# Optimization experiments

Measured on AMD Instinct MI355X. Metric: run time of the kernel, lower is better.

## Reference

```python
import jax, jax.numpy as jnp
import numpy as np

H = 32  # hidden_size

def _lstm_cell(x, h, c, Wih, Whh, bih, bhh):
    # PyTorch LSTMCell: gates order i, f, g, o
    g = x @ Wih.T + bih + h @ Whh.T + bhh  # [B, 4H]
    i, f, gg, o = jnp.split(g, 4, axis=-1)
    i = jax.nn.sigmoid(i); f = jax.nn.sigmoid(f)
    gg = jnp.tanh(gg);     o = jax.nn.sigmoid(o)
    c_new = f * c + i * gg
    h_new = o * jnp.tanh(c_new)
    return h_new, c_new


def setup_inputs() -> dict:
    key = jax.random.key(0)
    ks = jax.random.split(key, 16)
    B, T, I = 16384, 32, 27
    s_ih0 = 1.0 / np.sqrt(H)
    inp = {
        "obscured_tensor": jax.random.uniform(ks[0], (B, T, I), dtype=jnp.float32),
        "guessed_tensor": jax.random.uniform(ks[1], (B, 26), dtype=jnp.float32),
        # init_state uses xavier_normal on [B,H]: std = sqrt(2/(B+H))
        "h0": jax.random.normal(ks[2], (B, H), dtype=jnp.float32) * np.sqrt(2.0 / (B + H)),
        "c0": jax.random.normal(ks[3], (B, H), dtype=jnp.float32) * np.sqrt(2.0 / (B + H)),
        # layer 0 LSTMCell params (uniform(-1/sqrt(H), 1/sqrt(H)) like torch)
        "Wih0": jax.random.uniform(ks[4], (4 * H, I), jnp.float32, -s_ih0, s_ih0),
        "Whh0": jax.random.uniform(ks[5], (4 * H, H), jnp.float32, -s_ih0, s_ih0),
        "bih0": jax.random.uniform(ks[6], (4 * H,), jnp.float32, -s_ih0, s_ih0),
        "bhh0": jax.random.uniform(ks[7], (4 * H,), jnp.float32, -s_ih0, s_ih0),
        # layer 1 LSTMCell params
        "Wih1": jax.random.uniform(ks[8], (4 * H, H), jnp.float32, -s_ih0, s_ih0),
        "Whh1": jax.random.uniform(ks[9], (4 * H, H), jnp.float32, -s_ih0, s_ih0),
        "bih1": jax.random.uniform(ks[10], (4 * H,), jnp.float32, -s_ih0, s_ih0),
        "bhh1": jax.random.uniform(ks[11], (4 * H,), jnp.float32, -s_ih0, s_ih0),
        # fc: Linear(H + 26, 26)
        "Wfc": jax.random.uniform(ks[12], (26, H + 26), jnp.float32, -1.0 / np.sqrt(H + 26), 1.0 / np.sqrt(H + 26)),
        "bfc": jax.random.uniform(ks[13], (26,), jnp.float32, -1.0 / np.sqrt(H + 26), 1.0 / np.sqrt(H + 26)),
    }
    return inp


def reference(obscured_tensor, guessed_tensor, h0, c0,
              Wih0, Whh0, bih0, bhh0, Wih1, Whh1, bih1, bhh1, Wfc, bfc):
    B, T, _ = obscured_tensor.shape
    # faithful to torch: .view(T, B, -1) is a raw reshape, not a transpose
    xs = obscured_tensor.reshape(T, B, -1)  # [T, B, 27]

    def step(carry, x):
        h1, c1, h2, c2, hsum = carry
        h1, c1 = _lstm_cell(x, h1, c1, Wih0, Whh0, bih0, bhh0)
        h2, c2 = _lstm_cell(h1, h2, c2, Wih1, Whh1, bih1, bhh1)
        return (h1, c1, h2, c2, hsum + h2), None

    # init_state aliases the same xavier-initialized tensor for all layers
    init = (h0, c0, h0, c0, jnp.zeros_like(h0))
    (h1, c1, h2, c2, hsum), _ = jax.lax.scan(step, init, xs)

    # 'avg' aggregation: mean over time of concat(h_top, guessed);
    # guessed is time-constant so mean(concat) == concat(mean(h), guessed)
    agg = jnp.concatenate([hsum / T, guessed_tensor], axis=1)  # [B, H+26]
    logits = agg @ Wfc.T + bfc
    return logits, jax.nn.sigmoid(logits)
```

## Files before the change

kernel.cpp:

```cpp
#include <hip/hip_runtime.h>
#include <hip/hip_bf16.h>

#define NB 16384
#define NT 32
#define NI 27
#define NH 32
#define NG 26

typedef __attribute__((ext_vector_type(8))) short bf16x8;
typedef __attribute__((ext_vector_type(4))) float f32x4;
typedef __attribute__((ext_vector_type(4))) int   i32x4;

#define MFMA(a, b, c) __builtin_amdgcn_mfma_f32_16x16x32_bf16((a), (b), (c), 0, 0, 0)

static __device__ __forceinline__ int pack2(float lo, float hi) {
    unsigned short a = __builtin_bit_cast(unsigned short, __float2bfloat16(lo));
    unsigned short b = __builtin_bit_cast(unsigned short, __float2bfloat16(hi));
    return (int)(((unsigned)b << 16) | (unsigned)a);
}

static __device__ __forceinline__ float sigm(float x) {
    return __builtin_amdgcn_rcpf(1.0f + __expf(-x));
}
static __device__ __forceinline__ float tanh_(float x) {
    return 2.0f * __builtin_amdgcn_rcpf(1.0f + __expf(-2.0f * x)) - 1.0f;
}

static __device__ __forceinline__ bf16x8 load_wfrag(const float* __restrict__ W,
                                                    int rowlen, int nrows, int row, int k0) {
    int w[4];
#pragma unroll
    for (int q = 0; q < 4; ++q) {
        int k = k0 + 2 * q;
        float lo = (row < nrows && k     < rowlen) ? W[row * rowlen + k]     : 0.0f;
        float hi = (row < nrows && k + 1 < rowlen) ? W[row * rowlen + k + 1] : 0.0f;
        w[q] = pack2(lo, hi);
    }
    i32x4 v = { w[0], w[1], w[2], w[3] };
    return __builtin_bit_cast(bf16x8, v);
}

static __device__ __forceinline__ bf16x8 redist(const float hn[4][2], int a0, int a1, bool mhi) {
    int w00 = pack2(hn[0][0], hn[1][0]);
    int w01 = pack2(hn[2][0], hn[3][0]);
    int w10 = pack2(hn[0][1], hn[1][1]);
    int w11 = pack2(hn[2][1], hn[3][1]);
    int q0lo = __builtin_amdgcn_ds_bpermute(a0, w00), q0hi = __builtin_amdgcn_ds_bpermute(a0, w10);
    int q1lo = __builtin_amdgcn_ds_bpermute(a0, w01), q1hi = __builtin_amdgcn_ds_bpermute(a0, w11);
    int q2lo = __builtin_amdgcn_ds_bpermute(a1, w00), q2hi = __builtin_amdgcn_ds_bpermute(a1, w10);
    int q3lo = __builtin_amdgcn_ds_bpermute(a1, w01), q3hi = __builtin_amdgcn_ds_bpermute(a1, w11);
    i32x4 v = { mhi ? q0hi : q0lo, mhi ? q1hi : q1lo, mhi ? q2hi : q2lo, mhi ? q3hi : q3lo };
    return __builtin_bit_cast(bf16x8, v);
}

__global__ __launch_bounds__(256, 1)
void lstm_mfma(const float* __restrict__ X,
               const float* __restrict__ Gu,
               const float* __restrict__ H0, const float* __restrict__ C0,
               const float* __restrict__ Wih0, const float* __restrict__ Whh0,
               const float* __restrict__ bih0, const float* __restrict__ bhh0,
               const float* __restrict__ Wih1, const float* __restrict__ Whh1,
               const float* __restrict__ bih1, const float* __restrict__ bhh1,
               const float* __restrict__ Wfc, const float* __restrict__ bfc,
               float* __restrict__ out)
{
    const int lane = threadIdx.x & 63;
    const int bl   = lane & 15;
    const int g4   = lane >> 4;
    const int k0   = 8 * g4;
    const int wid  = blockIdx.x * (blockDim.x >> 6) + (threadIdx.x >> 6);
    const int batch = wid * 16 + bl;
    const bool mhi = (g4 >> 1) != 0;
    const int a0 = 4 * (bl + 16 * (2 * (g4 & 1)));
    const int a1 = a0 + 64;

    bf16x8 A0x[8], A0h[8], A1i[8], A1h[8];
    f32x4  b0[8], b1[8];
#pragma unroll
    for (int m = 0; m < 8; ++m) {
        A0x[m] = load_wfrag(Wih0, NI, 4 * NH, 16 * m + bl, k0);
        A0h[m] = load_wfrag(Whh0, NH, 4 * NH, 16 * m + bl, k0);
        A1i[m] = load_wfrag(Wih1, NH, 4 * NH, 16 * m + bl, k0);
        A1h[m] = load_wfrag(Whh1, NH, 4 * NH, 16 * m + bl, k0);
#pragma unroll
        for (int r = 0; r < 4; ++r) {
            int gr = 16 * m + 4 * g4 + r;
            b0[m][r] = bih0[gr] + bhh0[gr];
            b1[m][r] = bih1[gr] + bhh1[gr];
        }
    }
    bf16x8 Afc0[2], Afc1[2];
#pragma unroll
    for (int m2 = 0; m2 < 2; ++m2) {
        Afc0[m2] = load_wfrag(Wfc, NH + NG, NG, 16 * m2 + bl, k0);
        Afc1[m2] = load_wfrag(Wfc, NH + NG, NG, 16 * m2 + bl, NH + k0);
    }

    const float* h0p = H0 + (size_t)batch * NH;
    const float* c0p = C0 + (size_t)batch * NH;
    int hw[4];
#pragma unroll
    for (int q = 0; q < 4; ++q) hw[q] = pack2(h0p[k0 + 2 * q], h0p[k0 + 2 * q + 1]);
    i32x4 hv = { hw[0], hw[1], hw[2], hw[3] };
    bf16x8 h1f = __builtin_bit_cast(bf16x8, hv);
    bf16x8 h2f = h1f;
    float c1[4][2], c2[4][2], hsum[4][2];
#pragma unroll
    for (int mh = 0; mh < 2; ++mh)
#pragma unroll
        for (int r = 0; r < 4; ++r) {
            float c = c0p[16 * mh + 4 * g4 + r];
            c1[r][mh] = c; c2[r][mh] = c; hsum[r][mh] = 0.0f;
        }

    float xn[8];
    {
        const float* xp = X + ((size_t)0 * NB + batch) * NI;
#pragma unroll
        for (int j = 0; j < 8; ++j) { int k = k0 + j; xn[j] = (k < NI) ? xp[k] : 0.0f; }
    }

#pragma unroll 1
    for (int t = 0; t < NT; ++t) {
        int xw[4];
#pragma unroll
        for (int q = 0; q < 4; ++q) xw[q] = pack2(xn[2 * q], xn[2 * q + 1]);
        i32x4 xv = { xw[0], xw[1], xw[2], xw[3] };
        bf16x8 xf = __builtin_bit_cast(bf16x8, xv);
        if (t + 1 < NT) {
            const float* xp = X + ((size_t)(t + 1) * NB + batch) * NI;
#pragma unroll
            for (int j = 0; j < 8; ++j) { int k = k0 + j; xn[j] = (k < NI) ? xp[k] : 0.0f; }
        }

        f32x4 g[8];
#pragma unroll
        for (int m = 0; m < 8; ++m) g[m] = MFMA(A0x[m], xf, b0[m]);
#pragma unroll
        for (int m = 0; m < 8; ++m) g[m] = MFMA(A0h[m], h1f, g[m]);
        float hn1[4][2];
#pragma unroll
        for (int mh = 0; mh < 2; ++mh)
#pragma unroll
            for (int r = 0; r < 4; ++r) {
                float iv = sigm(g[0 + mh][r]);
                float fv = sigm(g[2 + mh][r]);
                float gv = tanh_(g[4 + mh][r]);
                float ov = sigm(g[6 + mh][r]);
                float c  = fmaf(fv, c1[r][mh], iv * gv);
                c1[r][mh] = c;
                hn1[r][mh] = ov * tanh_(c);
            }
        h1f = redist(hn1, a0, a1, mhi);

#pragma unroll
        for (int m = 0; m < 8; ++m) g[m] = MFMA(A1i[m], h1f, b1[m]);
#pragma unroll
        for (int m = 0; m < 8; ++m) g[m] = MFMA(A1h[m], h2f, g[m]);
        float hn2[4][2];
#pragma unroll
        for (int mh = 0; mh < 2; ++mh)
#pragma unroll
            for (int r = 0; r < 4; ++r) {
                float iv = sigm(g[0 + mh][r]);
                float fv = sigm(g[2 + mh][r]);
                float gv = tanh_(g[4 + mh][r]);
                float ov = sigm(g[6 + mh][r]);
                float c  = fmaf(fv, c2[r][mh], iv * gv);
                c2[r][mh] = c;
                float h = ov * tanh_(c);
                hn2[r][mh] = h;
                hsum[r][mh] += h;
            }
        h2f = redist(hn2, a0, a1, mhi);
    }

    float hs[4][2];
#pragma unroll
    for (int mh = 0; mh < 2; ++mh)
#pragma unroll
        for (int r = 0; r < 4; ++r) hs[r][mh] = hsum[r][mh] * (1.0f / NT);
    bf16x8 hsf = redist(hs, a0, a1, mhi);

    int gw[4];
    {
        const float* gp = Gu + (size_t)batch * NG;
#pragma unroll
        for (int q = 0; q < 4; ++q) {
            int k = k0 + 2 * q;
            float lo = (k     < NG) ? gp[k]     : 0.0f;
            float hi = (k + 1 < NG) ? gp[k + 1] : 0.0f;
            gw[q] = pack2(lo, hi);
        }
    }
    i32x4 gv_ = { gw[0], gw[1], gw[2], gw[3] };
    bf16x8 guf = __builtin_bit_cast(bf16x8, gv_);

    f32x4 zero4 = { 0.0f, 0.0f, 0.0f, 0.0f };
    f32x4 L[2];
#pragma unroll
    for (int m2 = 0; m2 < 2; ++m2) L[m2] = MFMA(Afc0[m2], hsf, zero4);
#pragma unroll
    for (int m2 = 0; m2 < 2; ++m2) L[m2] = MFMA(Afc1[m2], guf, L[m2]);

#pragma unroll
    for (int m2 = 0; m2 < 2; ++m2)
#pragma unroll
        for (int r = 0; r < 4; ++r) {
            int row = 16 * m2 + 4 * g4 + r;
            if (row < NG) {
                float v = L[m2][r] + bfc[row];
                out[(size_t)batch * NG + row] = v;
                out[(size_t)NB * NG + (size_t)batch * NG + row] = sigm(v);
            }
        }
}

extern "C" void kernel_launch(void* const* d_in, const int* in_sizes, int n_in,
                              void* d_out, int out_size, void* d_ws, size_t ws_size,
                              hipStream_t stream) {
    const float* X    = (const float*)d_in[0];
    const float* Gu   = (const float*)d_in[1];
    const float* H0   = (const float*)d_in[2];
    const float* C0   = (const float*)d_in[3];
    const float* Wih0 = (const float*)d_in[4];
    const float* Whh0 = (const float*)d_in[5];
    const float* bih0 = (const float*)d_in[6];
    const float* bhh0 = (const float*)d_in[7];
    const float* Wih1 = (const float*)d_in[8];
    const float* Whh1 = (const float*)d_in[9];
    const float* bih1 = (const float*)d_in[10];
    const float* bhh1 = (const float*)d_in[11];
    const float* Wfc  = (const float*)d_in[12];
    const float* bfc  = (const float*)d_in[13];
    float* out = (float*)d_out;

    dim3 grid(NB / 16 / 4), block(256);
    hipLaunchKernelGGL(lstm_mfma, grid, block, 0, stream,
                       X, Gu, H0, C0, Wih0, Whh0, bih0, bhh0,
                       Wih1, Whh1, bih1, bhh1, Wfc, bfc, out);
}
```

Measured before the change: 77.47 us.

## Split each 16-batch LSTM tile across two waves with LDS exchange

Each 16-row batch tile was handled by one wave computing all 8 gate row-blocks. It is now split across two waves that each compute 4 gate blocks, chosen so every wave holds one i/f/g/o block for its own 16 hidden units. The hidden state is exchanged through shared memory with a __syncthreads per layer per step, replacing the in-wave ds_bpermute redistribution. This doubles the wave count, from 1024 to 2048, and halves the per-wave serial MFMA and activation chain, to expose more parallelism. In exchange it adds block barriers and LDS round-trips on the recurrent critical path.

```diff
diff --git a/kernel.cpp b/kernel.cpp
--- a/kernel.cpp
+++ b/kernel.cpp
@@ -40,61 +40,44 @@
     return __builtin_bit_cast(bf16x8, v);
 }
 
-static __device__ __forceinline__ bf16x8 redist(const float hn[4][2], int a0, int a1, bool mhi) {
-    int w00 = pack2(hn[0][0], hn[1][0]);
-    int w01 = pack2(hn[2][0], hn[3][0]);
-    int w10 = pack2(hn[0][1], hn[1][1]);
-    int w11 = pack2(hn[2][1], hn[3][1]);
-    int q0lo = __builtin_amdgcn_ds_bpermute(a0, w00), q0hi = __builtin_amdgcn_ds_bpermute(a0, w10);
-    int q1lo = __builtin_amdgcn_ds_bpermute(a0, w01), q1hi = __builtin_amdgcn_ds_bpermute(a0, w11);
-    int q2lo = __builtin_amdgcn_ds_bpermute(a1, w00), q2hi = __builtin_amdgcn_ds_bpermute(a1, w10);
-    int q3lo = __builtin_amdgcn_ds_bpermute(a1, w01), q3hi = __builtin_amdgcn_ds_bpermute(a1, w11);
-    i32x4 v = { mhi ? q0hi : q0lo, mhi ? q1hi : q1lo, mhi ? q2hi : q2lo, mhi ? q3hi : q3lo };
-    return __builtin_bit_cast(bf16x8, v);
-}
-
-__global__ __launch_bounds__(256, 1)
-void lstm_mfma(const float* __restrict__ X,
-               const float* __restrict__ Gu,
-               const float* __restrict__ H0, const float* __restrict__ C0,
-               const float* __restrict__ Wih0, const float* __restrict__ Whh0,
-               const float* __restrict__ bih0, const float* __restrict__ bhh0,
-               const float* __restrict__ Wih1, const float* __restrict__ Whh1,
-               const float* __restrict__ bih1, const float* __restrict__ bhh1,
-               const float* __restrict__ Wfc, const float* __restrict__ bfc,
-               float* __restrict__ out)
+__global__ __launch_bounds__(128, 2)
+void lstm_split(const float* __restrict__ X,
+                const float* __restrict__ Gu,
+                const float* __restrict__ H0, const float* __restrict__ C0,
+                const float* __restrict__ Wih0, const float* __restrict__ Whh0,
+                const float* __restrict__ bih0, const float* __restrict__ bhh0,
+                const float* __restrict__ Wih1, const float* __restrict__ Whh1,
+                const float* __restrict__ bih1, const float* __restrict__ bhh1,
+                const float* __restrict__ Wfc, const float* __restrict__ bfc,
+                float* __restrict__ out)
 {
     const int lane = threadIdx.x & 63;
+    const int s    = threadIdx.x >> 6;
     const int bl   = lane & 15;
     const int g4   = lane >> 4;
     const int k0   = 8 * g4;
-    const int wid  = blockIdx.x * (blockDim.x >> 6) + (threadIdx.x >> 6);
-    const int batch = wid * 16 + bl;
-    const bool mhi = (g4 >> 1) != 0;
-    const int a0 = 4 * (bl + 16 * (2 * (g4 & 1)));
-    const int a1 = a0 + 64;
-
-    bf16x8 A0x[8], A0h[8], A1i[8], A1h[8];
-    f32x4  b0[8], b1[8];
-#pragma unroll
-    for (int m = 0; m < 8; ++m) {
-        A0x[m] = load_wfrag(Wih0, NI, 4 * NH, 16 * m + bl, k0);
-        A0h[m] = load_wfrag(Whh0, NH, 4 * NH, 16 * m + bl, k0);
-        A1i[m] = load_wfrag(Wih1, NH, 4 * NH, 16 * m + bl, k0);
-        A1h[m] = load_wfrag(Whh1, NH, 4 * NH, 16 * m + bl, k0);
+    const int batch = blockIdx.x * 16 + bl;
+
+    __shared__ unsigned int hb[2][16][16];
+
+    bf16x8 A0x[4], A0h[4], A1i[4], A1h[4];
+    f32x4  b0[4], b1[4];
+#pragma unroll
+    for (int j = 0; j < 4; ++j) {
+        int m = 2 * j + s;
+        A0x[j] = load_wfrag(Wih0, NI, 4 * NH, 16 * m + bl, k0);
+        A0h[j] = load_wfrag(Whh0, NH, 4 * NH, 16 * m + bl, k0);
+        A1i[j] = load_wfrag(Wih1, NH, 4 * NH, 16 * m + bl, k0);
+        A1h[j] = load_wfrag(Whh1, NH, 4 * NH, 16 * m + bl, k0);
 #pragma unroll
         for (int r = 0; r < 4; ++r) {
             int gr = 16 * m + 4 * g4 + r;
-            b0[m][r] = bih0[gr] + bhh0[gr];
-            b1[m][r] = bih1[gr] + bhh1[gr];
-        }
-    }
-    bf16x8 Afc0[2], Afc1[2];
-#pragma unroll
-    for (int m2 = 0; m2 < 2; ++m2) {
-        Afc0[m2] = load_wfrag(Wfc, NH + NG, NG, 16 * m2 + bl, k0);
-        Afc1[m2] = load_wfrag(Wfc, NH + NG, NG, 16 * m2 + bl, NH + k0);
-    }
+            b0[j][r] = bih0[gr] + bhh0[gr];
+            b1[j][r] = bih1[gr] + bhh1[gr];
+        }
+    }
+    bf16x8 Afc0 = load_wfrag(Wfc, NH + NG, NG, 16 * s + bl, k0);
+    bf16x8 Afc1 = load_wfrag(Wfc, NH + NG, NG, 16 * s + bl, NH + k0);
 
     const float* h0p = H0 + (size_t)batch * NH;
     const float* c0p = C0 + (size_t)batch * NH;
@@ -104,21 +87,21 @@
     i32x4 hv = { hw[0], hw[1], hw[2], hw[3] };
     bf16x8 h1f = __builtin_bit_cast(bf16x8, hv);
     bf16x8 h2f = h1f;
-    float c1[4][2], c2[4][2], hsum[4][2];
-#pragma unroll
-    for (int mh = 0; mh < 2; ++mh)
-#pragma unroll
-        for (int r = 0; r < 4; ++r) {
-            float c = c0p[16 * mh + 4 * g4 + r];
-            c1[r][mh] = c; c2[r][mh] = c; hsum[r][mh] = 0.0f;
-        }
+    float c1[4], c2[4], hsum[4];
+#pragma unroll
+    for (int r = 0; r < 4; ++r) {
+        float c = c0p[16 * s + 4 * g4 + r];
+        c1[r] = c; c2[r] = c; hsum[r] = 0.0f;
+    }
 
     float xn[8];
     {
-        const float* xp = X + ((size_t)0 * NB + batch) * NI;
+        const float* xp = X + (size_t)batch * NI;
 #pragma unroll
         for (int j = 0; j < 8; ++j) { int k = k0 + j; xn[j] = (k < NI) ? xp[k] : 0.0f; }
     }
+
+    const int wr = 8 * s + 2 * g4;
 
 #pragma unroll 1
     for (int t = 0; t < NT; ++t) {
@@ -133,54 +116,52 @@
             for (int j = 0; j < 8; ++j) { int k = k0 + j; xn[j] = (k < NI) ? xp[k] : 0.0f; }
         }
 
-        f32x4 g[8];
-#pragma unroll
-        for (int m = 0; m < 8; ++m) g[m] = MFMA(A0x[m], xf, b0[m]);
-#pragma unroll
-        for (int m = 0; m < 8; ++m) g[m] = MFMA(A0h[m], h1f, g[m]);
-        float hn1[4][2];
-#pragma unroll
-        for (int mh = 0; mh < 2; ++mh)
-#pragma unroll
-            for (int r = 0; r < 4; ++r) {
-                float iv = sigm(g[0 + mh][r]);
-                float fv = sigm(g[2 + mh][r]);
-                float gv = tanh_(g[4 + mh][r]);
-                float ov = sigm(g[6 + mh][r]);
-                float c  = fmaf(fv, c1[r][mh], iv * gv);
-                c1[r][mh] = c;
-                hn1[r][mh] = ov * tanh_(c);
-            }
-        h1f = redist(hn1, a0, a1, mhi);
-
-#pragma unroll
-        for (int m = 0; m < 8; ++m) g[m] = MFMA(A1i[m], h1f, b1[m]);
-#pragma unroll
-        for (int m = 0; m < 8; ++m) g[m] = MFMA(A1h[m], h2f, g[m]);
-        float hn2[4][2];
-#pragma unroll
-        for (int mh = 0; mh < 2; ++mh)
-#pragma unroll
-            for (int r = 0; r < 4; ++r) {
-                float iv = sigm(g[0 + mh][r]);
-                float fv = sigm(g[2 + mh][r]);
-                float gv = tanh_(g[4 + mh][r]);
-                float ov = sigm(g[6 + mh][r]);
-                float c  = fmaf(fv, c2[r][mh], iv * gv);
-                c2[r][mh] = c;
-                float h = ov * tanh_(c);
-                hn2[r][mh] = h;
-                hsum[r][mh] += h;
-            }
-        h2f = redist(hn2, a0, a1, mhi);
-    }
-
-    float hs[4][2];
-#pragma unroll
-    for (int mh = 0; mh < 2; ++mh)
-#pragma unroll
-        for (int r = 0; r < 4; ++r) hs[r][mh] = hsum[r][mh] * (1.0f / NT);
-    bf16x8 hsf = redist(hs, a0, a1, mhi);
+        f32x4 g[4];
+#pragma unroll
+        for (int j = 0; j < 4; ++j) g[j] = MFMA(A0x[j], xf, b0[j]);
+#pragma unroll
+        for (int j = 0; j < 4; ++j) g[j] = MFMA(A0h[j], h1f, g[j]);
+        float hn[4];
+#pragma unroll
+        for (int r = 0; r < 4; ++r) {
+            float iv = sigm(g[0][r]);
+            float fv = sigm(g[1][r]);
+            float gv = tanh_(g[2][r]);
+            float ov = sigm(g[3][r]);
+            c1[r] = fmaf(fv, c1[r], iv * gv);
+            hn[r] = ov * tanh_(c1[r]);
+        }
+        *(uint2*)&hb[0][bl][wr] = make_uint2((unsigned)pack2(hn[0], hn[1]),
+                                             (unsigned)pack2(hn[2], hn[3]));
+        __syncthreads();
+        h1f = __builtin_bit_cast(bf16x8, *(const i32x4*)&hb[0][bl][4 * g4]);
+
+#pragma unroll
+        for (int j = 0; j < 4; ++j) g[j] = MFMA(A1i[j], h1f, b1[j]);
+#pragma unroll
+        for (int j = 0; j < 4; ++j) g[j] = MFMA(A1h[j], h2f, g[j]);
+#pragma unroll
+        for (int r = 0; r < 4; ++r) {
+            float iv = sigm(g[0][r]);
+            float fv = sigm(g[1][r]);
+            float gv = tanh_(g[2][r]);
+            float ov = sigm(g[3][r]);
+            c2[r] = fmaf(fv, c2[r], iv * gv);
+            float h = ov * tanh_(c2[r]);
+            hn[r] = h;
+            hsum[r] += h;
+        }
+        *(uint2*)&hb[1][bl][wr] = make_uint2((unsigned)pack2(hn[0], hn[1]),
+                                             (unsigned)pack2(hn[2], hn[3]));
+        __syncthreads();
+        h2f = __builtin_bit_cast(bf16x8, *(const i32x4*)&hb[1][bl][4 * g4]);
+    }
+
+    *(uint2*)&hb[0][bl][wr] = make_uint2(
+        (unsigned)pack2(hsum[0] * (1.0f / NT), hsum[1] * (1.0f / NT)),
+        (unsigned)pack2(hsum[2] * (1.0f / NT), hsum[3] * (1.0f / NT)));
+    __syncthreads();
+    bf16x8 hsf = __builtin_bit_cast(bf16x8, *(const i32x4*)&hb[0][bl][4 * g4]);
 
     int gw[4];
     {
@@ -197,23 +178,18 @@
     bf16x8 guf = __builtin_bit_cast(bf16x8, gv_);
 
     f32x4 zero4 = { 0.0f, 0.0f, 0.0f, 0.0f };
-    f32x4 L[2];
-#pragma unroll
-    for (int m2 = 0; m2 < 2; ++m2) L[m2] = MFMA(Afc0[m2], hsf, zero4);
-#pragma unroll
-    for (int m2 = 0; m2 < 2; ++m2) L[m2] = MFMA(Afc1[m2], guf, L[m2]);
-
-#pragma unroll
-    for (int m2 = 0; m2 < 2; ++m2)
-#pragma unroll
-        for (int r = 0; r < 4; ++r) {
-            int row = 16 * m2 + 4 * g4 + r;
-            if (row < NG) {
-                float v = L[m2][r] + bfc[row];
-                out[(size_t)batch * NG + row] = v;
-                out[(size_t)NB * NG + (size_t)batch * NG + row] = sigm(v);
-            }
-        }
+    f32x4 L = MFMA(Afc0, hsf, zero4);
+    L = MFMA(Afc1, guf, L);
+
+#pragma unroll
+    for (int r = 0; r < 4; ++r) {
+        int row = 16 * s + 4 * g4 + r;
+        if (row < NG) {
+            float v = L[r] + bfc[row];
+            out[(size_t)batch * NG + row] = v;
+            out[(size_t)NB * NG + (size_t)batch * NG + row] = sigm(v);
+        }
+    }
 }
 
 extern "C" void kernel_launch(void* const* d_in, const int* in_sizes, int n_in,
@@ -235,8 +211,8 @@
     const float* bfc  = (const float*)d_in[13];
     float* out = (float*)d_out;
 
-    dim3 grid(NB / 16 / 4), block(256);
-    hipLaunchKernelGGL(lstm_mfma, grid, block, 0, stream,
+    dim3 grid(NB / 16), block(128);
+    hipLaunchKernelGGL(lstm_split, grid, block, 0, stream,
                        X, Gu, H0, C0, Wih0, Whh0, bih0, bhh0,
                        Wih1, Whh1, bih1, bhh1, Wfc, bfc, out);
 }
```

Measured after the change: 89.34 us. +15.3%, slower.

## Software-pipeline layer-0 gate MFMAs of next step with layer-1 activations

Applied to the files above, without the earlier changes.

Restructures the time loop so the layer-0 gate matrix multiplies for step t+1 are issued right after the layer-1 MFMAs for step t, before the layer-1 activation math runs. This lets MFMA work overlap with the transcendental activation VALU work and breaks the strict serial dependency chain within each step. The input prefetch distance grows to two steps, and a second gate accumulator set adds register pressure.

```diff
diff --git a/kernel.cpp b/kernel.cpp
--- a/kernel.cpp
+++ b/kernel.cpp
@@ -54,7 +54,7 @@
 }
 
 __global__ __launch_bounds__(256, 1)
-void lstm_mfma(const float* __restrict__ X,
+void lstm_pipe(const float* __restrict__ X,
                const float* __restrict__ Gu,
                const float* __restrict__ H0, const float* __restrict__ C0,
                const float* __restrict__ Wih0, const float* __restrict__ Whh0,
@@ -114,58 +114,83 @@
         }
 
     float xn[8];
+    bf16x8 xf;
     {
-        const float* xp = X + ((size_t)0 * NB + batch) * NI;
-#pragma unroll
-        for (int j = 0; j < 8; ++j) { int k = k0 + j; xn[j] = (k < NI) ? xp[k] : 0.0f; }
-    }
+        const float* xp = X + (size_t)batch * NI;
+        int xw[4];
+#pragma unroll
+        for (int q = 0; q < 4; ++q) {
+            int k = k0 + 2 * q;
+            float lo = (k     < NI) ? xp[k]     : 0.0f;
+            float hi = (k + 1 < NI) ? xp[k + 1] : 0.0f;
+            xw[q] = pack2(lo, hi);
+        }
+        i32x4 xv = { xw[0], xw[1], xw[2], xw[3] };
+        xf = __builtin_bit_cast(bf16x8, xv);
+        const float* xp1 = X + ((size_t)NB + batch) * NI;
+#pragma unroll
+        for (int j = 0; j < 8; ++j) { int k = k0 + j; xn[j] = (k < NI) ? xp1[k] : 0.0f; }
+    }
+
+    f32x4 gL0[8];
+#pragma unroll
+    for (int m = 0; m < 8; ++m) gL0[m] = MFMA(A0x[m], xf, b0[m]);
+#pragma unroll
+    for (int m = 0; m < 8; ++m) gL0[m] = MFMA(A0h[m], h1f, gL0[m]);
 
 #pragma unroll 1
     for (int t = 0; t < NT; ++t) {
-        int xw[4];
-#pragma unroll
-        for (int q = 0; q < 4; ++q) xw[q] = pack2(xn[2 * q], xn[2 * q + 1]);
-        i32x4 xv = { xw[0], xw[1], xw[2], xw[3] };
-        bf16x8 xf = __builtin_bit_cast(bf16x8, xv);
-        if (t + 1 < NT) {
-            const float* xp = X + ((size_t)(t + 1) * NB + batch) * NI;
-#pragma unroll
-            for (int j = 0; j < 8; ++j) { int k = k0 + j; xn[j] = (k < NI) ? xp[k] : 0.0f; }
-        }
-
-        f32x4 g[8];
-#pragma unroll
-        for (int m = 0; m < 8; ++m) g[m] = MFMA(A0x[m], xf, b0[m]);
-#pragma unroll
-        for (int m = 0; m < 8; ++m) g[m] = MFMA(A0h[m], h1f, g[m]);
         float hn1[4][2];
 #pragma unroll
         for (int mh = 0; mh < 2; ++mh)
 #pragma unroll
             for (int r = 0; r < 4; ++r) {
-                float iv = sigm(g[0 + mh][r]);
-                float fv = sigm(g[2 + mh][r]);
-                float gv = tanh_(g[4 + mh][r]);
-                float ov = sigm(g[6 + mh][r]);
+                float iv = sigm(gL0[0 + mh][r]);
+                float fv = sigm(gL0[2 + mh][r]);
+                float gv = tanh_(gL0[4 + mh][r]);
+                float ov = sigm(gL0[6 + mh][r]);
                 float c  = fmaf(fv, c1[r][mh], iv * gv);
                 c1[r][mh] = c;
                 hn1[r][mh] = ov * tanh_(c);
             }
         h1f = redist(hn1, a0, a1, mhi);
 
-#pragma unroll
-        for (int m = 0; m < 8; ++m) g[m] = MFMA(A1i[m], h1f, b1[m]);
-#pragma unroll
-        for (int m = 0; m < 8; ++m) g[m] = MFMA(A1h[m], h2f, g[m]);
+        {
+            int xw[4];
+#pragma unroll
+            for (int q = 0; q < 4; ++q) xw[q] = pack2(xn[2 * q], xn[2 * q + 1]);
+            i32x4 xv = { xw[0], xw[1], xw[2], xw[3] };
+            xf = __builtin_bit_cast(bf16x8, xv);
+        }
+
+        f32x4 gL1[8];
+#pragma unroll
+        for (int m = 0; m < 8; ++m) gL1[m] = MFMA(A1i[m], h1f, b1[m]);
+#pragma unroll
+        for (int m = 0; m < 8; ++m) gL1[m] = MFMA(A1h[m], h2f, gL1[m]);
+
+        if (t + 1 < NT) {
+#pragma unroll
+            for (int m = 0; m < 8; ++m) gL0[m] = MFMA(A0x[m], xf, b0[m]);
+#pragma unroll
+            for (int m = 0; m < 8; ++m) gL0[m] = MFMA(A0h[m], h1f, gL0[m]);
+        }
+
+        if (t + 2 < NT) {
+            const float* xp = X + ((size_t)(t + 2) * NB + batch) * NI;
+#pragma unroll
+            for (int j = 0; j < 8; ++j) { int k = k0 + j; xn[j] = (k < NI) ? xp[k] : 0.0f; }
+        }
+
         float hn2[4][2];
 #pragma unroll
         for (int mh = 0; mh < 2; ++mh)
 #pragma unroll
             for (int r = 0; r < 4; ++r) {
-                float iv = sigm(g[0 + mh][r]);
-                float fv = sigm(g[2 + mh][r]);
-                float gv = tanh_(g[4 + mh][r]);
-                float ov = sigm(g[6 + mh][r]);
+                float iv = sigm(gL1[0 + mh][r]);
+                float fv = sigm(gL1[2 + mh][r]);
+                float gv = tanh_(gL1[4 + mh][r]);
+                float ov = sigm(gL1[6 + mh][r]);
                 float c  = fmaf(fv, c2[r][mh], iv * gv);
                 c2[r][mh] = c;
                 float h = ov * tanh_(c);
@@ -236,7 +261,7 @@
     float* out = (float*)d_out;
 
     dim3 grid(NB / 16 / 4), block(256);
-    hipLaunchKernelGGL(lstm_mfma, grid, block, 0, stream,
+    hipLaunchKernelGGL(lstm_pipe, grid, block, 0, stream,
                        X, Gu, H0, C0, Wih0, Whh0, bih0, bhh0,
                        Wih1, Whh1, bih1, bhh1, Wfc, bfc, out);
 }
```

After: 79.89 us. 3.1% more time.

## Split LSTM layers across two wavefronts in a software pipeline

Applied to the files above, without the earlier changes.

Each block now handles 16 batch rows with two wavefronts. Wave 0 runs layer 0 and wave 1 runs layer 1 one timestep behind, and layer-0 hidden state is handed over through a double-buffered LDS slot with a block barrier every step. Each wave holds half the weight fragments, which frees registers and lets more waves run at once. The two layers' serial dependency chains can then overlap. In exchange it adds 33 __syncthreads per block, one extra pipeline step, and grows the grid from 256 to 1024 blocks.

```diff
diff --git a/kernel.cpp b/kernel.cpp
--- a/kernel.cpp
+++ b/kernel.cpp
@@ -53,47 +53,45 @@
     return __builtin_bit_cast(bf16x8, v);
 }
 
-__global__ __launch_bounds__(256, 1)
-void lstm_mfma(const float* __restrict__ X,
-               const float* __restrict__ Gu,
-               const float* __restrict__ H0, const float* __restrict__ C0,
-               const float* __restrict__ Wih0, const float* __restrict__ Whh0,
-               const float* __restrict__ bih0, const float* __restrict__ bhh0,
-               const float* __restrict__ Wih1, const float* __restrict__ Whh1,
-               const float* __restrict__ bih1, const float* __restrict__ bhh1,
-               const float* __restrict__ Wfc, const float* __restrict__ bfc,
-               float* __restrict__ out)
+__global__ __launch_bounds__(128, 2)
+void lstm_ws(const float* __restrict__ X,
+             const float* __restrict__ Gu,
+             const float* __restrict__ H0, const float* __restrict__ C0,
+             const float* __restrict__ Wih0, const float* __restrict__ Whh0,
+             const float* __restrict__ bih0, const float* __restrict__ bhh0,
+             const float* __restrict__ Wih1, const float* __restrict__ Whh1,
+             const float* __restrict__ bih1, const float* __restrict__ bhh1,
+             const float* __restrict__ Wfc, const float* __restrict__ bfc,
+             float* __restrict__ out)
 {
     const int lane = threadIdx.x & 63;
+    const int s    = threadIdx.x >> 6;
     const int bl   = lane & 15;
     const int g4   = lane >> 4;
     const int k0   = 8 * g4;
-    const int wid  = blockIdx.x * (blockDim.x >> 6) + (threadIdx.x >> 6);
-    const int batch = wid * 16 + bl;
+    const int batch = blockIdx.x * 16 + bl;
     const bool mhi = (g4 >> 1) != 0;
     const int a0 = 4 * (bl + 16 * (2 * (g4 & 1)));
     const int a1 = a0 + 64;
 
-    bf16x8 A0x[8], A0h[8], A1i[8], A1h[8];
-    f32x4  b0[8], b1[8];
+    __shared__ i32x4 hls[2][64];
+
+    const float* Wxp = s ? Wih1 : Wih0;  const int xlen = s ? NH : NI;
+    const float* Whp = s ? Whh1 : Whh0;
+    const float* bip = s ? bih1 : bih0;
+    const float* bhp = s ? bhh1 : bhh0;
+
+    bf16x8 Wxf[8], Whf[8];
+    f32x4  bias[8];
 #pragma unroll
     for (int m = 0; m < 8; ++m) {
-        A0x[m] = load_wfrag(Wih0, NI, 4 * NH, 16 * m + bl, k0);
-        A0h[m] = load_wfrag(Whh0, NH, 4 * NH, 16 * m + bl, k0);
-        A1i[m] = load_wfrag(Wih1, NH, 4 * NH, 16 * m + bl, k0);
-        A1h[m] = load_wfrag(Whh1, NH, 4 * NH, 16 * m + bl, k0);
+        Wxf[m] = load_wfrag(Wxp, xlen, 4 * NH, 16 * m + bl, k0);
+        Whf[m] = load_wfrag(Whp, NH,   4 * NH, 16 * m + bl, k0);
 #pragma unroll
         for (int r = 0; r < 4; ++r) {
             int gr = 16 * m + 4 * g4 + r;
-            b0[m][r] = bih0[gr] + bhh0[gr];
-            b1[m][r] = bih1[gr] + bhh1[gr];
-        }
-    }
-    bf16x8 Afc0[2], Afc1[2];
-#pragma unroll
-    for (int m2 = 0; m2 < 2; ++m2) {
-        Afc0[m2] = load_wfrag(Wfc, NH + NG, NG, 16 * m2 + bl, k0);
-        Afc1[m2] = load_wfrag(Wfc, NH + NG, NG, 16 * m2 + bl, NH + k0);
+            bias[m][r] = bip[gr] + bhp[gr];
+        }
     }
 
     const float* h0p = H0 + (size_t)batch * NH;
@@ -102,88 +100,88 @@
 #pragma unroll
     for (int q = 0; q < 4; ++q) hw[q] = pack2(h0p[k0 + 2 * q], h0p[k0 + 2 * q + 1]);
     i32x4 hv = { hw[0], hw[1], hw[2], hw[3] };
-    bf16x8 h1f = __builtin_bit_cast(bf16x8, hv);
-    bf16x8 h2f = h1f;
-    float c1[4][2], c2[4][2], hsum[4][2];
+    bf16x8 hfrag = __builtin_bit_cast(bf16x8, hv);
+    float cst[4][2], hsum[4][2];
 #pragma unroll
     for (int mh = 0; mh < 2; ++mh)
 #pragma unroll
         for (int r = 0; r < 4; ++r) {
-            float c = c0p[16 * mh + 4 * g4 + r];
-            c1[r][mh] = c; c2[r][mh] = c; hsum[r][mh] = 0.0f;
+            cst[r][mh] = c0p[16 * mh + 4 * g4 + r];
+            hsum[r][mh] = 0.0f;
         }
 
     float xn[8];
-    {
-        const float* xp = X + ((size_t)0 * NB + batch) * NI;
+    if (s == 0) {
+        const float* xp = X + (size_t)batch * NI;
 #pragma unroll
         for (int j = 0; j < 8; ++j) { int k = k0 + j; xn[j] = (k < NI) ? xp[k] : 0.0f; }
     }
 
+    bf16x8 Afc0[2], Afc1[2];
+    if (s) {
+#pragma unroll
+        for (int m2 = 0; m2 < 2; ++m2) {
+            Afc0[m2] = load_wfrag(Wfc, NH + NG, NG, 16 * m2 + bl, k0);
+            Afc1[m2] = load_wfrag(Wfc, NH + NG, NG, 16 * m2 + bl, NH + k0);
+        }
+    }
+
 #pragma unroll 1
-    for (int t = 0; t < NT; ++t) {
-        int xw[4];
-#pragma unroll
-        for (int q = 0; q < 4; ++q) xw[q] = pack2(xn[2 * q], xn[2 * q + 1]);
-        i32x4 xv = { xw[0], xw[1], xw[2], xw[3] };
-        bf16x8 xf = __builtin_bit_cast(bf16x8, xv);
-        if (t + 1 < NT) {
-            const float* xp = X + ((size_t)(t + 1) * NB + batch) * NI;
-#pragma unroll
-            for (int j = 0; j < 8; ++j) { int k = k0 + j; xn[j] = (k < NI) ? xp[k] : 0.0f; }
-        }
-
-        f32x4 g[8];
-#pragma unroll
-        for (int m = 0; m < 8; ++m) g[m] = MFMA(A0x[m], xf, b0[m]);
-#pragma unroll
-        for (int m = 0; m < 8; ++m) g[m] = MFMA(A0h[m], h1f, g[m]);
-        float hn1[4][2];
+    for (int it = 0; it <= NT; ++it) {
+        const bool active = s ? (it >= 1) : (it < NT);
+        if (active) {
+            bf16x8 in;
+            if (s == 0) {
+                int xw[4];
+#pragma unroll
+                for (int q = 0; q < 4; ++q) xw[q] = pack2(xn[2 * q], xn[2 * q + 1]);
+                i32x4 xv = { xw[0], xw[1], xw[2], xw[3] };
+                in = __builtin_bit_cast(bf16x8, xv);
+                if (it + 1 < NT) {
+                    const float* xp = X + ((size_t)(it + 1) * NB + batch) * NI;
+#pragma unroll
+                    for (int j = 0; j < 8; ++j) { int k = k0 + j; xn[j] = (k < NI) ? xp[k] : 0.0f; }
+                }
+            } else {
+                in = __builtin_bit_cast(bf16x8, hls[(it - 1) & 1][lane]);
+            }
+
+            f32x4 g[8];
+#pragma unroll
+            for (int m = 0; m < 8; ++m) g[m] = MFMA(Whf[m], hfrag, bias[m]);
+#pragma unroll
+            for (int m = 0; m < 8; ++m) g[m] = MFMA(Wxf[m], in, g[m]);
+
+            float hn[4][2];
+#pragma unroll
+            for (int mh = 0; mh < 2; ++mh)
+#pragma unroll
+                for (int r = 0; r < 4; ++r) {
+                    float iv = sigm(g[0 + mh][r]);
+                    float fv = sigm(g[2 + mh][r]);
+                    float gv = tanh_(g[4 + mh][r]);
+                    float ov = sigm(g[6 + mh][r]);
+                    float c  = fmaf(fv, cst[r][mh], iv * gv);
+                    cst[r][mh] = c;
+                    float h = ov * tanh_(c);
+                    hn[r][mh] = h;
+                    hsum[r][mh] += h;
+                }
+            hfrag = redist(hn, a0, a1, mhi);
+            if (s == 0) hls[it & 1][lane] = __builtin_bit_cast(i32x4, hfrag);
+        }
+        __syncthreads();
+    }
+
+    if (s) {
+        float hs[4][2];
 #pragma unroll
         for (int mh = 0; mh < 2; ++mh)
 #pragma unroll
-            for (int r = 0; r < 4; ++r) {
-                float iv = sigm(g[0 + mh][r]);
-                float fv = sigm(g[2 + mh][r]);
-                float gv = tanh_(g[4 + mh][r]);
-                float ov = sigm(g[6 + mh][r]);
-                float c  = fmaf(fv, c1[r][mh], iv * gv);
-                c1[r][mh] = c;
-                hn1[r][mh] = ov * tanh_(c);
-            }
-        h1f = redist(hn1, a0, a1, mhi);
-
-#pragma unroll
-        for (int m = 0; m < 8; ++m) g[m] = MFMA(A1i[m], h1f, b1[m]);
-#pragma unroll
-        for (int m = 0; m < 8; ++m) g[m] = MFMA(A1h[m], h2f, g[m]);
-        float hn2[4][2];
-#pragma unroll
-        for (int mh = 0; mh < 2; ++mh)
-#pragma unroll
-            for (int r = 0; r < 4; ++r) {
-                float iv = sigm(g[0 + mh][r]);
-                float fv = sigm(g[2 + mh][r]);
-                float gv = tanh_(g[4 + mh][r]);
-                float ov = sigm(g[6 + mh][r]);
-                float c  = fmaf(fv, c2[r][mh], iv * gv);
-                c2[r][mh] = c;
-                float h = ov * tanh_(c);
-                hn2[r][mh] = h;
-                hsum[r][mh] += h;
-            }
-        h2f = redist(hn2, a0, a1, mhi);
-    }
-
-    float hs[4][2];
-#pragma unroll
-    for (int mh = 0; mh < 2; ++mh)
-#pragma unroll
-        for (int r = 0; r < 4; ++r) hs[r][mh] = hsum[r][mh] * (1.0f / NT);
-    bf16x8 hsf = redist(hs, a0, a1, mhi);
-
-    int gw[4];
-    {
+            for (int r = 0; r < 4; ++r) hs[r][mh] = hsum[r][mh] * (1.0f / NT);
+        bf16x8 hsf = redist(hs, a0, a1, mhi);
+
+        int gw[4];
         const float* gp = Gu + (size_t)batch * NG;
 #pragma unroll
         for (int q = 0; q < 4; ++q) {
@@ -192,28 +190,28 @@
             float hi = (k + 1 < NG) ? gp[k + 1] : 0.0f;
             gw[q] = pack2(lo, hi);
         }
-    }
-    i32x4 gv_ = { gw[0], gw[1], gw[2], gw[3] };
-    bf16x8 guf = __builtin_bit_cast(bf16x8, gv_);
-
-    f32x4 zero4 = { 0.0f, 0.0f, 0.0f, 0.0f };
-    f32x4 L[2];
-#pragma unroll
-    for (int m2 = 0; m2 < 2; ++m2) L[m2] = MFMA(Afc0[m2], hsf, zero4);
-#pragma unroll
-    for (int m2 = 0; m2 < 2; ++m2) L[m2] = MFMA(Afc1[m2], guf, L[m2]);
-
-#pragma unroll
-    for (int m2 = 0; m2 < 2; ++m2)
-#pragma unroll
-        for (int r = 0; r < 4; ++r) {
-            int row = 16 * m2 + 4 * g4 + r;
-            if (row < NG) {
-                float v = L[m2][r] + bfc[row];
-                out[(size_t)batch * NG + row] = v;
-                out[(size_t)NB * NG + (size_t)batch * NG + row] = sigm(v);
+        i32x4 gv_ = { gw[0], gw[1], gw[2], gw[3] };
+        bf16x8 guf = __builtin_bit_cast(bf16x8, gv_);
+
+        f32x4 zero4 = { 0.0f, 0.0f, 0.0f, 0.0f };
+        f32x4 L[2];
+#pragma unroll
+        for (int m2 = 0; m2 < 2; ++m2) L[m2] = MFMA(Afc0[m2], hsf, zero4);
+#pragma unroll
+        for (int m2 = 0; m2 < 2; ++m2) L[m2] = MFMA(Afc1[m2], guf, L[m2]);
+
+#pragma unroll
+        for (int m2 = 0; m2 < 2; ++m2)
+#pragma unroll
+            for (int r = 0; r < 4; ++r) {
+                int row = 16 * m2 + 4 * g4 + r;
+                if (row < NG) {
+                    float v = L[m2][r] + bfc[row];
+                    out[(size_t)batch * NG + row] = v;
+                    out[(size_t)NB * NG + (size_t)batch * NG + row] = sigm(v);
+                }
             }
-        }
+    }
 }
 
 extern "C" void kernel_launch(void* const* d_in, const int* in_sizes, int n_in,
@@ -235,8 +233,8 @@
     const float* bfc  = (const float*)d_in[13];
     float* out = (float*)d_out;
 
-    dim3 grid(NB / 16 / 4), block(256);
-    hipLaunchKernelGGL(lstm_mfma, grid, block, 0, stream,
+    dim3 grid(NB / 16), block(128);
+    hipLaunchKernelGGL(lstm_ws, grid, block, 0, stream,
                        X, Gu, H0, C0, Wih0, Whh0, bih0, bhh0,
                        Wih1, Whh1, bih1, bhh1, Wfc, bfc, out);
 }
```

New measurement: 76.81 us. No clear change (-0.9%).
